# Kernel tuning notes

Measured on AMD Instinct MI355X. Metric: run time of the kernel, lower is better.

Reference implementation:

```python
import jax, jax.numpy as jnp
import numpy as np

B, T, D, H, L, OUT, FC = 256, 512, 64, 256, 2, 1, 128


def setup_inputs() -> dict:
    key = jax.random.key(0)
    ks = jax.random.split(key, 16)
    s = 1.0 / np.sqrt(H)
    u = lambda k, shape: jax.random.uniform(k, shape, jnp.float32, -s, s)
    return {
        "x": jax.random.normal(ks[0], (B, T, D), jnp.float32),
        # layer 0 LSTM params (PyTorch gate order: i, f, g, o)
        "W_ih0": u(ks[1], (4 * H, D)),
        "W_hh0": u(ks[2], (4 * H, H)),
        "b_ih0": u(ks[3], (4 * H,)),
        "b_hh0": u(ks[4], (4 * H,)),
        # layer 1 LSTM params
        "W_ih1": u(ks[5], (4 * H, H)),
        "W_hh1": u(ks[6], (4 * H, H)),
        "b_ih1": u(ks[7], (4 * H,)),
        "b_hh1": u(ks[8], (4 * H,)),
        # MLP head
        "fc1_w": u(ks[9], (FC, H)),
        "fc1_b": u(ks[10], (FC,)),
        "fc2_w": u(ks[11], (OUT, FC)),
        "fc2_b": u(ks[12], (OUT,)),
    }


def _lstm_layer(x, W_ih, W_hh, b_ih, b_hh):
    # x: [B, T, Din] -> (outputs [B, T, H], final hidden [B, H])
    Bsz = x.shape[0]
    Hh = W_hh.shape[1]
    # precompute input contribution to all gates: [B, T, 4H]
    xg = jnp.einsum("btd,gd->btg", x, W_ih) + b_ih + b_hh

    def step(carry, xt):
        h, c = carry
        g = xt + h @ W_hh.T  # [B, 4H]
        i, f, gg, o = jnp.split(g, 4, axis=-1)
        i = jax.nn.sigmoid(i)
        f = jax.nn.sigmoid(f)
        gg = jnp.tanh(gg)
        o = jax.nn.sigmoid(o)
        c = f * c + i * gg
        h = o * jnp.tanh(c)
        return (h, c), h

    h0 = jnp.zeros((Bsz, Hh), x.dtype)
    (hT, _cT), hs = jax.lax.scan(step, (h0, h0), jnp.swapaxes(xg, 0, 1))
    return jnp.swapaxes(hs, 0, 1), hT


def reference(x, W_ih0, W_hh0, b_ih0, b_hh0, W_ih1, W_hh1, b_ih1, b_hh1,
              fc1_w, fc1_b, fc2_w, fc2_b):
    # eval-mode forward: inter-layer dropout (p=0.2) is a no-op
    y0, h0f = _lstm_layer(x, W_ih0, W_hh0, b_ih0, b_hh0)
    _y1, h1f = _lstm_layer(y0, W_ih1, W_hh1, b_ih1, b_hh1)
    # h_n.view(-1, H): stack per-layer final hidden states -> [L*B, H]
    h_n = jnp.concatenate([h0f, h1f], axis=0)
    out = jax.nn.relu(h_n)
    out = jax.nn.relu(out @ fc1_w.T + fc1_b)
    return out @ fc2_w.T + fc2_b  # [L*B, OUT]
```

## Files before the change

### kernel.cpp

```cpp
#include <hip/hip_runtime.h>

#define Bb 256
#define Tt 512
#define Dd 64
#define Hh 256
#define NP 16
#define HB2 (256 * 256)

typedef unsigned short u16;
typedef _Float16 f16;
typedef __attribute__((ext_vector_type(8))) _Float16 f16x8;
typedef __attribute__((ext_vector_type(4))) _Float16 f16x4;
typedef __attribute__((ext_vector_type(4))) float f32x4;
typedef __attribute__((ext_vector_type(4))) unsigned int u32x4;

__device__ __forceinline__ f16x8 bc8h(u32x4 v) { return __builtin_bit_cast(f16x8, v); }

__device__ __forceinline__ float fsig(float x) {
  x = fminf(fmaxf(x, -30.f), 30.f);
  return 1.f / (1.f + __expf(-x));
}
__device__ __forceinline__ float ftanh(float x) {
  x = fminf(fmaxf(x, -15.f), 15.f);
  float t = __expf(2.f * x);
  return (t - 1.f) / (t + 1.f);
}

__device__ __forceinline__ f16x8 ld16_sc1(const f16* p) {
  f16x8 r;
  asm volatile("global_load_dwordx4 %0, %1, off sc1" : "=v"(r) : "v"(p) : "memory");
  return r;
}
__device__ __forceinline__ f16x8 ld16_sc0(const f16* p) {
  f16x8 r;
  asm volatile("global_load_dwordx4 %0, %1, off sc0" : "=v"(r) : "v"(p) : "memory");
  return r;
}
__device__ __forceinline__ void st4_sc1(f16* p, unsigned v) {
  asm volatile("global_store_dword %0, %1, off sc1" : : "v"(p), "v"(v) : "memory");
}
__device__ __forceinline__ void st4_plain(f16* p, unsigned v) {
  asm volatile("global_store_dword %0, %1, off" : : "v"(p), "v"(v) : "memory");
}
__device__ __forceinline__ void st4u_plain(unsigned* p, unsigned v) {
  asm volatile("global_store_dword %0, %1, off" : : "v"(p), "v"(v) : "memory");
}
__device__ __forceinline__ void st4u_sc1(unsigned* p, unsigned v) {
  asm volatile("global_store_dword %0, %1, off sc1" : : "v"(p), "v"(v) : "memory");
}
__device__ __forceinline__ unsigned ld4_sc0(const unsigned* p) {
  unsigned r;
  asm volatile("global_load_dword %0, %1, off sc0\n\ts_waitcnt vmcnt(0)"
               : "=v"(r) : "v"(p) : "memory");
  return r;
}

__global__ __launch_bounds__(256) void prep_x(const float* __restrict__ x,
                                              f16* __restrict__ xh) {
  int i = blockIdx.x * blockDim.x + threadIdx.x;
  const int n4 = Bb * Tt * Dd / 4;
  if (i >= n4) return;
  f32x4 v = ((const f32x4*)x)[i];
  f16x4 o;
#pragma unroll
  for (int j = 0; j < 4; ++j) o[j] = (f16)v[j];
  ((f16x4*)xh)[i] = o;
}

__global__ __launch_bounds__(256) void prep_w(
    const float* __restrict__ wih0, const float* __restrict__ whh0,
    const float* __restrict__ bih0, const float* __restrict__ bhh0,
    const float* __restrict__ wih1, const float* __restrict__ whh1,
    const float* __restrict__ bih1, const float* __restrict__ bhh1,
    f16* __restrict__ wfrag, float* __restrict__ bias0s, float* __restrict__ bias1s) {
  int tid = blockIdx.x * blockDim.x + threadIdx.x;
  int np = gridDim.x * blockDim.x;
  const int tot = 16 * 8 * 32 * 512;
  for (int u = tid; u < tot; u += np) {
    int e = u & 7, l = (u >> 3) & 63;
    int f = (u >> 9) & 31;
    int wv = (u >> 14) & 7;
    int p = u >> 17;
    int g = wv & 3;
    int grow = g * 256 + p * 16 + (l & 15);
    int klane = (l >> 4) * 8 + e;
    float w = 0.f;
    if (wv < 4) {
      if (f < 4)       w = wih0[grow * 64 + (f >> 1) * 32 + klane];
      else if (f < 20) w = whh0[grow * 256 + ((f - 4) >> 1) * 32 + klane];
    } else {
      if (f < 16)      w = wih1[grow * 256 + (f >> 1) * 32 + klane];
      else             w = whh1[grow * 256 + ((f - 16) >> 1) * 32 + klane];
    }
    f16 hi = (f16)w;
    wfrag[u] = (f & 1) ? (f16)((w - (float)hi) * 2048.0f) : hi;
  }
  for (int u = tid; u < 1024; u += np) {
    bias0s[u] = bih0[u] + bhh0[u];
    bias1s[u] = bih1[u] + bhh1[u];
  }
}

#define MF(A, B, C) __builtin_amdgcn_mfma_f32_16x16x32_f16(A, B, C, 0, 0, 0)

__global__ __launch_bounds__(512, 2) void lstm_persist(
    const f16* __restrict__ xh, const f16* __restrict__ wfrag,
    const float* __restrict__ bias0s, const float* __restrict__ bias1s,
    f16* h0, f16* h1, unsigned* flags, unsigned* probe, unsigned* verdict) {
  const int bid = blockIdx.x;
  const int p = (bid >> 3) & 15;
  const int grp = (bid & 7) * 2 + (bid >> 7);
  const int tid = threadIdx.x;
  const int wv = tid >> 6, lane = tid & 63;
  const int lr = lane & 15, lk = lane >> 4;
  const int g = wv & 3;
  const bool isL1 = wv >= 4;
  const float LOSCALE = 1.0f / 2048.0f;

  __shared__ float gbuf[2][4][16][16];
  __shared__ u32x4 hbuf[2][16][36];
  __shared__ unsigned s_fast;

  f16x8 wf[32];
  {
    const u32x4* wp = (const u32x4*)wfrag + ((size_t)(p * 8 + wv) * 32) * 64 + lane;
#pragma unroll
    for (int f = 0; f < 20; ++f) wf[f] = bc8h(wp[(size_t)f * 64]);
    if (isL1) {
#pragma unroll
      for (int f = 20; f < 32; ++f) wf[f] = bc8h(wp[(size_t)f * 64]);
    }
  }
  const float bias = (isL1 ? bias1s : bias0s)[g * 256 + p * 16 + lr];

  if (tid < 256) {
    int lsel = tid >> 7;
    int d = tid & 127;
    int row = d >> 3, cp = d & 7;
    f16* base = lsel ? h1 : (h0 + (size_t)3 * HB2);
    unsigned* w = (unsigned*)(base + (size_t)(grp * 16 + row) * 256 + p * 16) + cp;
    st4u_plain(w, 0u);
    st4u_sc1(w, 0u);
  }
  asm volatile("s_waitcnt vmcnt(0)" ::: "memory");
  __syncthreads();

  if (wv == 0) {
    if (lane == 0) {
      st4u_plain(&probe[grp * NP + p], (unsigned)(p + 1));
      asm volatile("s_waitcnt vmcnt(0)" ::: "memory");
    }
    bool seen = (lane >= NP);
    bool ok;
    int it = 0;
    while (true) {
      if (!seen) {
        unsigned got = ld4_sc0(&probe[grp * NP + lane]);
        if (got == (unsigned)(lane + 1)) seen = true;
      }
      if (__all(seen)) { ok = true; break; }
      if (++it > 768) { ok = false; break; }
      __builtin_amdgcn_s_sleep(2);
    }
    if (lane == 0)
      __hip_atomic_store(&verdict[grp * NP + p], ok ? 1u : 2u, __ATOMIC_RELAXED,
                         __HIP_MEMORY_SCOPE_AGENT);
    unsigned v;
    while (true) {
      v = 1u;
      if (lane < NP)
        v = __hip_atomic_load(&verdict[grp * NP + lane], __ATOMIC_RELAXED,
                              __HIP_MEMORY_SCOPE_AGENT);
      if (!__any(v == 0u)) break;
      __builtin_amdgcn_s_sleep(2);
    }
    if (lane == 0) s_fast = __any(v != 1u) ? 0u : 1u;
  }
  __syncthreads();
  const bool fast = (s_fast != 0u);

  float c0 = 0.f, c1 = 0.f;
  const int hrow = grp * 16 + lr;
  const f16* xbase = xh + (size_t)hrow * Tt * Dd + lk * 8;
  const f16* hsrcbase = ((wv < 4) ? h0 : h1) + (size_t)grp * 4096;
  const int hlsel = wv >> 2;

  for (int k = 0; k <= Tt; ++k) {
    f32x4 a = (f32x4){bias, bias, bias, bias};
    f32x4 b = (f32x4){0.f, 0.f, 0.f, 0.f};
    if (!isL1 && k < Tt) {
      const u32x4* xp = (const u32x4*)(xbase + (size_t)k * Dd);
      f16x8 xf0 = bc8h(xp[0]);
      f16x8 xf1 = bc8h(xp[4]);
      a = MF(xf0, wf[0], a);
      b = MF(xf0, wf[1], b);
      a = MF(xf1, wf[2], a);
      b = MF(xf1, wf[3], b);
    }

    if (wv == 0) {
      bool ready = false;
      while (!ready) {
        unsigned v = 0xFFFFFFFFu;
        if (lane < NP)
          v = __hip_atomic_load(&flags[grp * NP + lane], __ATOMIC_RELAXED,
                                __HIP_MEMORY_SCOPE_AGENT);
        ready = !__any(v < (unsigned)k);
        if (!ready) __builtin_amdgcn_s_sleep(1);
      }
    }
    asm volatile("" ::: "memory");
    __syncthreads();

    const int par = (k - 1) & 3;

    {
      const f16* src = hsrcbase + (size_t)par * HB2;
      const int j0 = (wv & 3) * 2;
      const f16* p0 = src + j0 * 512 + lane * 8;
      f16x8 s0, s1;
      if (fast) {
        s0 = ld16_sc0(p0);
        s1 = ld16_sc0(p0 + 512);
      } else {
        s0 = ld16_sc1(p0);
        s1 = ld16_sc1(p0 + 512);
      }
      asm volatile("s_waitcnt vmcnt(0)" ::: "memory");
      const int r0 = j0 * 2 + (lane >> 5);
      const int c = lane & 31;
      hbuf[hlsel][r0][c ^ (r0 & 7)] = __builtin_bit_cast(u32x4, s0);
      hbuf[hlsel][r0 + 2][c ^ ((r0 + 2) & 7)] = __builtin_bit_cast(u32x4, s1);
    }
    __syncthreads();

    f16x8 A0[8], A1[8];
#pragma unroll
    for (int kt = 0; kt < 8; ++kt)
      A0[kt] = __builtin_bit_cast(f16x8, hbuf[0][lr][(kt * 4 + lk) ^ (lr & 7)]);
    if (isL1) {
#pragma unroll
      for (int kt = 0; kt < 8; ++kt)
        A1[kt] = __builtin_bit_cast(f16x8, hbuf[1][lr][(kt * 4 + lk) ^ (lr & 7)]);
    }

    if (!isL1) {
      if (k < Tt) {
#pragma unroll
        for (int kt = 0; kt < 8; ++kt) {
          a = MF(A0[kt], wf[4 + 2 * kt], a);
          b = MF(A0[kt], wf[5 + 2 * kt], b);
        }
        a += b * LOSCALE;
#pragma unroll
        for (int r = 0; r < 4; ++r) gbuf[0][g][lk * 4 + r][lr] = a[r];
      }
    } else if (k >= 1) {
#pragma unroll
      for (int kt = 0; kt < 8; ++kt) {
        a = MF(A0[kt], wf[2 * kt], a);
        b = MF(A0[kt], wf[2 * kt + 1], b);
      }
#pragma unroll
      for (int kt = 0; kt < 8; ++kt) {
        a = MF(A1[kt], wf[16 + 2 * kt], a);
        b = MF(A1[kt], wf[17 + 2 * kt], b);
      }
      a += b * LOSCALE;
#pragma unroll
      for (int r = 0; r < 4; ++r) gbuf[1][g][lk * 4 + r][lr] = a[r];
    }
    __syncthreads();

    {
      const bool upd = ((wv & 2) == 0) && (isL1 ? (k >= 1) : (k < Tt));
      if (upd) {
        const int L = isL1 ? 1 : 0;
        int id0 = (wv & 1) * 128 + lane * 2;
        int row = id0 >> 4, col = id0 & 15;
        float iv = fsig(gbuf[L][0][row][col]);
        float fv = fsig(gbuf[L][1][row][col]);
        float gv = ftanh(gbuf[L][2][row][col]);
        float ov = fsig(gbuf[L][3][row][col]);
        c0 = fv * c0 + iv * gv;
        float ha = ov * ftanh(c0);
        iv = fsig(gbuf[L][0][row][col + 1]);
        fv = fsig(gbuf[L][1][row][col + 1]);
        gv = ftanh(gbuf[L][2][row][col + 1]);
        ov = fsig(gbuf[L][3][row][col + 1]);
        c1 = fv * c1 + iv * gv;
        float hb = ov * ftanh(c1);
        f16 fa = (f16)ha, fb = (f16)hb;
        unsigned pack = (unsigned)__builtin_bit_cast(u16, fa) |
                        ((unsigned)__builtin_bit_cast(u16, fb) << 16);
        f16* Ho = (isL1 ? h1 : h0) + (size_t)(k & 3) * HB2 +
                  (grp * 16 + row) * 256 + p * 16 + col;
        if (fast) st4_plain(Ho, pack);
        else      st4_sc1(Ho, pack);
      }
    }
    asm volatile("s_waitcnt vmcnt(0)" ::: "memory");
    __syncthreads();
    if (tid == 0)
      __hip_atomic_store(&flags[grp * NP + p], (unsigned)(k + 1), __ATOMIC_RELAXED,
                         __HIP_MEMORY_SCOPE_AGENT);
  }
}

__global__ __launch_bounds__(128) void head_kernel(
    const f16* __restrict__ h0f, const f16* __restrict__ h1f,
    const float* __restrict__ fc1w, const float* __restrict__ fc1b,
    const float* __restrict__ fc2w, const float* __restrict__ fc2b,
    float* __restrict__ out) {
  int r = blockIdx.x;
  const f16* hh = (r < 256) ? (h0f + r * Hh) : (h1f + (r - 256) * Hh);
  __shared__ float v[Hh];
  int tid = threadIdx.x;
  for (int i = tid; i < Hh; i += 128)
    v[i] = fmaxf((float)hh[i], 0.f);
  __syncthreads();
  float s = fc1b[tid];
#pragma unroll 8
  for (int i = 0; i < Hh; ++i) s += fc1w[tid * Hh + i] * v[i];
  s = fmaxf(s, 0.f) * fc2w[tid];
#pragma unroll
  for (int off = 32; off; off >>= 1) s += __shfl_down(s, off);
  __shared__ float red[2];
  if ((tid & 63) == 0) red[tid >> 6] = s;
  __syncthreads();
  if (tid == 0) out[r] = red[0] + red[1] + fc2b[0];
}

extern "C" void kernel_launch(void* const* d_in, const int* in_sizes, int n_in,
                              void* d_out, int out_size, void* d_ws, size_t ws_size,
                              hipStream_t stream) {
  (void)in_sizes; (void)n_in; (void)out_size; (void)ws_size;
  const float* x    = (const float*)d_in[0];
  const float* wih0 = (const float*)d_in[1];
  const float* whh0 = (const float*)d_in[2];
  const float* bih0 = (const float*)d_in[3];
  const float* bhh0 = (const float*)d_in[4];
  const float* wih1 = (const float*)d_in[5];
  const float* whh1 = (const float*)d_in[6];
  const float* bih1 = (const float*)d_in[7];
  const float* bhh1 = (const float*)d_in[8];
  const float* fc1w = (const float*)d_in[9];
  const float* fc1b = (const float*)d_in[10];
  const float* fc2w = (const float*)d_in[11];
  const float* fc2b = (const float*)d_in[12];

  char* ws = (char*)d_ws;
  size_t off = 0;
  f16* xh = (f16*)(ws + off); off += (size_t)Bb * Tt * Dd * 2;
  f16* wfrag = (f16*)(ws + off); off += (size_t)16 * 8 * 32 * 512 * 2;
  float* bias0s = (float*)(ws + off); off += 4096;
  float* bias1s = (float*)(ws + off); off += 4096;
  char* zbase = ws + off;
  f16* h0 = (f16*)(ws + off); off += (size_t)4 * HB2 * 2;
  f16* h1 = (f16*)(ws + off); off += (size_t)4 * HB2 * 2;
  unsigned* flags = (unsigned*)(ws + off); off += 1024;
  unsigned* probe = (unsigned*)(ws + off); off += 1024;
  unsigned* verdict = (unsigned*)(ws + off); off += 1024;
  size_t zbytes = (size_t)((ws + off) - zbase);

  hipMemsetAsync(zbase, 0, zbytes, stream);
  prep_x<<<Bb * Tt * Dd / 4 / 256, 256, 0, stream>>>(x, xh);
  prep_w<<<512, 256, 0, stream>>>(wih0, whh0, bih0, bhh0, wih1, whh1, bih1, bhh1,
                                  wfrag, bias0s, bias1s);
  lstm_persist<<<256, 512, 0, stream>>>(xh, wfrag, bias0s, bias1s, h0, h1, flags,
                                        probe, verdict);
  head_kernel<<<512, 128, 0, stream>>>(h0 + (size_t)3 * HB2, h1, fc1w, fc1b,
                                       fc2w, fc2b, (float*)d_out);
}
```

Measured before the change: 1.720 ms.

## Poll L2-resident step flags and spread gate update across all threads

Adds a second flag array written with plain stores and polled with sc0 loads in fast mode, so inter-block step polling can be served from L2 instead of agent-scope atomics. It falls back to the atomic flags every 64 spins. The elementwise LSTM cell update is also spread from 4 waves doing two elements each to all 512 threads doing one element each, storing halfwords. This shortens the serial per-step critical path, at the cost of extra flag stores and narrower, more numerous global stores.

```diff
diff --git a/kernel.cpp b/kernel.cpp
--- a/kernel.cpp
+++ b/kernel.cpp
@@ -36,11 +36,11 @@
   asm volatile("global_load_dwordx4 %0, %1, off sc0" : "=v"(r) : "v"(p) : "memory");
   return r;
 }
-__device__ __forceinline__ void st4_sc1(f16* p, unsigned v) {
-  asm volatile("global_store_dword %0, %1, off sc1" : : "v"(p), "v"(v) : "memory");
-}
-__device__ __forceinline__ void st4_plain(f16* p, unsigned v) {
-  asm volatile("global_store_dword %0, %1, off" : : "v"(p), "v"(v) : "memory");
+__device__ __forceinline__ void st2_sc1(f16* p, unsigned v) {
+  asm volatile("global_store_short %0, %1, off sc1" : : "v"(p), "v"(v) : "memory");
+}
+__device__ __forceinline__ void st2_plain(f16* p, unsigned v) {
+  asm volatile("global_store_short %0, %1, off" : : "v"(p), "v"(v) : "memory");
 }
 __device__ __forceinline__ void st4u_plain(unsigned* p, unsigned v) {
   asm volatile("global_store_dword %0, %1, off" : : "v"(p), "v"(v) : "memory");
@@ -106,7 +106,8 @@
 __global__ __launch_bounds__(512, 2) void lstm_persist(
     const f16* __restrict__ xh, const f16* __restrict__ wfrag,
     const float* __restrict__ bias0s, const float* __restrict__ bias1s,
-    f16* h0, f16* h1, unsigned* flags, unsigned* probe, unsigned* verdict) {
+    f16* h0, f16* h1, unsigned* flags, unsigned* flagsL2, unsigned* probe,
+    unsigned* verdict) {
   const int bid = blockIdx.x;
   const int p = (bid >> 3) & 15;
   const int grp = (bid & 7) * 2 + (bid >> 7);
@@ -142,6 +143,7 @@
     st4u_plain(w, 0u);
     st4u_sc1(w, 0u);
   }
+  if (tid == 0) st4u_plain(&flagsL2[grp * NP + p], 0u);
   asm volatile("s_waitcnt vmcnt(0)" ::: "memory");
   __syncthreads();
 
@@ -179,7 +181,11 @@
   __syncthreads();
   const bool fast = (s_fast != 0u);
 
-  float c0 = 0.f, c1 = 0.f;
+  const int eL = tid >> 8;
+  const int erow = (tid >> 4) & 15, ecol = tid & 15;
+  float c = 0.f;
+  f16* const hout = ((eL ? h1 : h0) + (size_t)(grp * 16 + erow) * 256 + p * 16 + ecol);
+
   const int hrow = grp * 16 + lr;
   const f16* xbase = xh + (size_t)hrow * Tt * Dd + lk * 8;
   const f16* hsrcbase = ((wv < 4) ? h0 : h1) + (size_t)grp * 4096;
@@ -199,14 +205,31 @@
     }
 
     if (wv == 0) {
+      int spin = 0;
       bool ready = false;
       while (!ready) {
         unsigned v = 0xFFFFFFFFu;
-        if (lane < NP)
-          v = __hip_atomic_load(&flags[grp * NP + lane], __ATOMIC_RELAXED,
-                                __HIP_MEMORY_SCOPE_AGENT);
+        if (lane < NP) {
+          if (fast) {
+            v = ld4_sc0(&flagsL2[grp * NP + lane]);
+          } else {
+            v = __hip_atomic_load(&flags[grp * NP + lane], __ATOMIC_RELAXED,
+                                  __HIP_MEMORY_SCOPE_AGENT);
+          }
+        }
         ready = !__any(v < (unsigned)k);
-        if (!ready) __builtin_amdgcn_s_sleep(1);
+        if (!ready) {
+          ++spin;
+          if (fast && (spin & 63) == 0 && lane < NP) {
+            unsigned v3 = __hip_atomic_load(&flags[grp * NP + lane],
+                                            __ATOMIC_RELAXED,
+                                            __HIP_MEMORY_SCOPE_AGENT);
+            ready = false;
+            v = v > v3 ? v : v3;
+          }
+          ready = !__any(v < (unsigned)k);
+          if (!ready) __builtin_amdgcn_s_sleep(1);
+        }
       }
     }
     asm volatile("" ::: "memory");
@@ -228,9 +251,9 @@
       }
       asm volatile("s_waitcnt vmcnt(0)" ::: "memory");
       const int r0 = j0 * 2 + (lane >> 5);
-      const int c = lane & 31;
-      hbuf[hlsel][r0][c ^ (r0 & 7)] = __builtin_bit_cast(u32x4, s0);
-      hbuf[hlsel][r0 + 2][c ^ ((r0 + 2) & 7)] = __builtin_bit_cast(u32x4, s1);
+      const int c2 = lane & 31;
+      hbuf[hlsel][r0][c2 ^ (r0 & 7)] = __builtin_bit_cast(u32x4, s0);
+      hbuf[hlsel][r0 + 2][c2 ^ ((r0 + 2) & 7)] = __builtin_bit_cast(u32x4, s1);
     }
     __syncthreads();
 
@@ -273,37 +296,29 @@
     __syncthreads();
 
     {
-      const bool upd = ((wv & 2) == 0) && (isL1 ? (k >= 1) : (k < Tt));
+      const bool upd = eL ? (k >= 1) : (k < Tt);
       if (upd) {
-        const int L = isL1 ? 1 : 0;
-        int id0 = (wv & 1) * 128 + lane * 2;
-        int row = id0 >> 4, col = id0 & 15;
-        float iv = fsig(gbuf[L][0][row][col]);
-        float fv = fsig(gbuf[L][1][row][col]);
-        float gv = ftanh(gbuf[L][2][row][col]);
-        float ov = fsig(gbuf[L][3][row][col]);
-        c0 = fv * c0 + iv * gv;
-        float ha = ov * ftanh(c0);
-        iv = fsig(gbuf[L][0][row][col + 1]);
-        fv = fsig(gbuf[L][1][row][col + 1]);
-        gv = ftanh(gbuf[L][2][row][col + 1]);
-        ov = fsig(gbuf[L][3][row][col + 1]);
-        c1 = fv * c1 + iv * gv;
-        float hb = ov * ftanh(c1);
-        f16 fa = (f16)ha, fb = (f16)hb;
-        unsigned pack = (unsigned)__builtin_bit_cast(u16, fa) |
-                        ((unsigned)__builtin_bit_cast(u16, fb) << 16);
-        f16* Ho = (isL1 ? h1 : h0) + (size_t)(k & 3) * HB2 +
-                  (grp * 16 + row) * 256 + p * 16 + col;
-        if (fast) st4_plain(Ho, pack);
-        else      st4_sc1(Ho, pack);
+        float iv = fsig(gbuf[eL][0][erow][ecol]);
+        float fv = fsig(gbuf[eL][1][erow][ecol]);
+        float gv = ftanh(gbuf[eL][2][erow][ecol]);
+        float ov = fsig(gbuf[eL][3][erow][ecol]);
+        c = fv * c + iv * gv;
+        float hval = ov * ftanh(c);
+        f16 fh = (f16)hval;
+        unsigned bits = (unsigned)__builtin_bit_cast(u16, fh);
+        f16* Ho = hout + (size_t)(k & 3) * HB2;
+        if (fast) st2_plain(Ho, bits);
+        else      st2_sc1(Ho, bits);
       }
     }
     asm volatile("s_waitcnt vmcnt(0)" ::: "memory");
     __syncthreads();
-    if (tid == 0)
-      __hip_atomic_store(&flags[grp * NP + p], (unsigned)(k + 1), __ATOMIC_RELAXED,
+    if (tid == 0) {
+      unsigned nv = (unsigned)(k + 1);
+      if (fast) st4u_plain(&flagsL2[grp * NP + p], nv);
+      __hip_atomic_store(&flags[grp * NP + p], nv, __ATOMIC_RELAXED,
                          __HIP_MEMORY_SCOPE_AGENT);
+    }
   }
 }
 
@@ -359,6 +374,7 @@
   f16* h0 = (f16*)(ws + off); off += (size_t)4 * HB2 * 2;
   f16* h1 = (f16*)(ws + off); off += (size_t)4 * HB2 * 2;
   unsigned* flags = (unsigned*)(ws + off); off += 1024;
+  unsigned* flagsL2 = (unsigned*)(ws + off); off += 1024;
   unsigned* probe = (unsigned*)(ws + off); off += 1024;
   unsigned* verdict = (unsigned*)(ws + off); off += 1024;
   size_t zbytes = (size_t)((ws + off) - zbase);
@@ -368,7 +384,7 @@
   prep_w<<<512, 256, 0, stream>>>(wih0, whh0, bih0, bhh0, wih1, whh1, bih1, bhh1,
                                   wfrag, bias0s, bias1s);
   lstm_persist<<<256, 512, 0, stream>>>(xh, wfrag, bias0s, bias1s, h0, h1, flags,
-                                        probe, verdict);
+                                        flagsL2, probe, verdict);
   head_kernel<<<512, 128, 0, stream>>>(h0 + (size_t)3 * HB2, h1, fc1w, fc1b,
                                        fc2w, fc2b, (float*)d_out);
 }
```

After: 5.114 ms. +197.3%, slower.
